# Kernel optimization log

Hardware: AMD Instinct MI355X
Metric: run time of the kernel (lower is better)

## Reference

```python
import jax, jax.numpy as jnp
import numpy as np

N_SUBJECTS, C_IN, C_OUT = 128, 273, 273
B, T = 256, 360


def setup_inputs() -> dict:
    key = jax.random.key(0)
    k1, k2, k3 = jax.random.split(key, 3)
    x = jax.random.normal(k1, (B, C_IN, T), dtype=jnp.float32)
    subjects = jax.random.randint(k2, (B,), 0, N_SUBJECTS, dtype=jnp.int64)
    weights = jax.random.normal(k3, (N_SUBJECTS, C_IN, C_OUT), dtype=jnp.float32)
    return {"x": x, "subjects": subjects, "weights": weights}


def reference(x, subjects, weights):
    # Gather per-sample weight matrix: (B, C, D)
    w = weights[subjects]
    # bct,bcd -> bdt : per-sample channel remap applied at every timestep
    return jnp.einsum('bct,bcd->bdt', x, w)
```

## Files before the change

kernel.cpp:

```cpp
#include <hip/hip_runtime.h>
#include <hip/hip_bf16.h>

#define NBATCH 256
#define NC 273
#define ND 273
#define NT 360
#define NSUB 128

#define THREADS 512
#define BM 288
#define BN 192
#define BK 32
#define LDK 40
#define KITERS 9

#define WT_LD 288
#define WT_SUBJ (288 * 288)
#define WT_BYTES ((size_t)NSUB * WT_SUBJ * 2)

typedef __bf16 bf16_t;
typedef bf16_t bf16x4 __attribute__((ext_vector_type(4)));
typedef bf16_t bf16x8 __attribute__((ext_vector_type(8)));
typedef float  f32x4  __attribute__((ext_vector_type(4)));

#define LDS_FENCE_BARRIER()                                   \
    do {                                                      \
        asm volatile("s_waitcnt lgkmcnt(0)" ::: "memory");    \
        __builtin_amdgcn_s_barrier();                         \
    } while (0)

__global__ __launch_bounds__(256) void conv_w(const float* __restrict__ w,
                                              bf16_t* __restrict__ wT) {
    const int bid  = blockIdx.x;
    const int s    = bid / 25;
    const int tile = bid % 25;
    const int c0   = (tile / 5) * 64;
    const int d0   = (tile % 5) * 64;
    const int tx   = threadIdx.x & 63;
    const int ty   = threadIdx.x >> 6;

    __shared__ float t[64][65];
    const float* __restrict__ wsrc = w + (size_t)s * NC * ND;
#pragma unroll
    for (int j = 0; j < 16; ++j) {
        const int row = ty + j * 4;
        const int c = c0 + row, d = d0 + tx;
        t[row][tx] = (c < NC && d < ND) ? wsrc[c * ND + d] : 0.f;
    }
    __syncthreads();
    bf16_t* __restrict__ wdst = wT + (size_t)s * WT_SUBJ;
#pragma unroll
    for (int j = 0; j < 16; ++j) {
        const int row = ty + j * 4;
        const int d = d0 + row, c = c0 + tx;
        if (d < ND && c < WT_LD)
            wdst[d * WT_LD + c] = (bf16_t)t[tx][row];
    }
}

template<bool BF16W>
__global__ __launch_bounds__(THREADS, 2) void subject_gemm(
    const float*  __restrict__ x,
    const int*    __restrict__ subjects,
    const float*  __restrict__ w,
    const bf16_t* __restrict__ wT,
    float*        __restrict__ out)
{
    const int raw  = blockIdx.x;
    const int xcd  = raw & 7;
    const int slot = raw >> 3;
    const int b    = xcd * 32 + (slot >> 1);
    const int tt   = slot & 1;
    const int t0   = tt * BN;
    const int bnv  = tt ? (NT - BN) : BN;
    const int s    = subjects[b];

    const float*  __restrict__ xb  = x  + (size_t)b * NC * NT;
    const float*  __restrict__ wsf = w  + (size_t)s * NC * ND;
    const bf16_t* __restrict__ wsb = wT + (size_t)s * WT_SUBJ;

    __shared__ __align__(16) bf16_t As[2][BM * LDK];
    __shared__ __align__(16) bf16_t Bs[2][BN * LDK];

    const int tid   = threadIdx.x;
    const int lane  = tid & 63;
    const int wid   = tid >> 6;
    const int wm    = wid >> 2;
    const int wn    = wid & 3;
    const int l16   = lane & 15;
    const int khalf = lane >> 4;

    int offA[5], gA[5], dA[5], cqA[5];
#pragma unroll
    for (int j = 0; j < 5; ++j) {
        const int i  = tid + THREADS * j;
        const int ii = (i < 2304) ? i : 2303;
        const int kq = ii & 7;
        const int d  = ii >> 3;
        offA[j] = d * LDK + kq * 4;
        gA[j]   = d * WT_LD + kq * 4;
        dA[j]   = d;
        cqA[j]  = kq * 4;
    }
    int offB[3], gB[3];
#pragma unroll
    for (int j = 0; j < 3; ++j) {
        const int i  = tid + THREADS * j;
        const int t  = i % BN;
        const int kq = i / BN;
        const int tc = (t < bnv) ? t : (bnv - 1);
        offB[j] = t * LDK + kq * 4;
        gB[j]   = kq * 4 * NT + t0 + tc;
    }
    const bool haveJ4 = (tid < 2304 - 4 * THREADS);

    bf16x4 aEv[5], aOd[5];
    float  bEv[3][4], bOd[3][4];

    auto loadA = [&](bf16x4 (&r)[5], int kk) {
        if constexpr (BF16W) {
#pragma unroll
            for (int j = 0; j < 4; ++j)
                r[j] = *(const bf16x4*)&wsb[gA[j] + kk];
            if (haveJ4)
                r[4] = *(const bf16x4*)&wsb[gA[4] + kk];
        } else {
#pragma unroll
            for (int j = 0; j < 5; ++j) {
                if (j == 4 && !haveJ4) break;
                bf16x4 v;
#pragma unroll
                for (int u = 0; u < 4; ++u) {
                    const int c = kk + cqA[j] + u;
                    const float f = (c < NC && dA[j] < ND) ? wsf[c * ND + dA[j]] : 0.f;
                    v[u] = (bf16_t)f;
                }
                r[j] = v;
            }
        }
    };
    auto loadB = [&](float (&r)[3][4], int kk) {
        const int base = kk * NT;
#pragma unroll
        for (int j = 0; j < 3; ++j)
#pragma unroll
            for (int u = 0; u < 4; ++u)
                r[j][u] = xb[base + gB[j] + u * NT];
    };
    auto loadB_tail = [&](float (&r)[3][4]) {
#pragma unroll
        for (int j = 0; j < 3; ++j) {
#pragma unroll
            for (int u = 0; u < 4; ++u) {
                const int c  = 256 + (gB[j] / NT)  + u;
                const int cc = (c < NC) ? c : (NC - 1);
                r[j][u] = xb[cc * NT + (gB[j] % NT)];
            }
        }
    };
    auto stage = [&](const bf16x4 (&rA)[5], const float (&rB)[3][4],
                     bf16_t* dA_, bf16_t* dB_) {
#pragma unroll
        for (int j = 0; j < 4; ++j)
            *(bf16x4*)&dA_[offA[j]] = rA[j];
        if (haveJ4)
            *(bf16x4*)&dA_[offA[4]] = rA[4];
#pragma unroll
        for (int j = 0; j < 3; ++j) {
            bf16x4 v;
#pragma unroll
            for (int u = 0; u < 4; ++u) v[u] = (bf16_t)rB[j][u];
            *(bf16x4*)&dB_[offB[j]] = v;
        }
    };

    f32x4 acc[9][3];
#pragma unroll
    for (int m = 0; m < 9; ++m)
#pragma unroll
        for (int n = 0; n < 3; ++n)
            acc[m][n] = (f32x4){0.f, 0.f, 0.f, 0.f};

    loadA(aEv, 0);       loadB(bEv, 0);
    loadA(aOd, BK);      loadB(bOd, BK);
    stage(aEv, bEv, &As[0][0], &Bs[0][0]);
    LDS_FENCE_BARRIER();

#pragma unroll
    for (int p = 0; p < 4; ++p) {
        {
            const int it0 = 2 * p;
            bf16x8 af[9], bfr[3];
#pragma unroll
            for (int n = 0; n < 3; ++n)
                bfr[n] = *(const bf16x8*)&Bs[0][(wn * 48 + n * 16 + l16) * LDK + khalf * 8];
#pragma unroll
            for (int m = 0; m < 9; ++m)
                af[m] = *(const bf16x8*)&As[0][(wm * 144 + m * 16 + l16) * LDK + khalf * 8];

            if (it0 + 2 <= KITERS - 2) {
                loadA(aEv, (it0 + 2) * BK);
                loadB(bEv, (it0 + 2) * BK);
            } else {
                loadA(aEv, 256);
                loadB_tail(bEv);
            }
            stage(aOd, bOd, &As[1][0], &Bs[1][0]);
            LDS_FENCE_BARRIER();

#pragma unroll
            for (int m = 0; m < 9; ++m)
#pragma unroll
                for (int n = 0; n < 3; ++n)
                    acc[m][n] = __builtin_amdgcn_mfma_f32_16x16x32_bf16(af[m], bfr[n], acc[m][n], 0, 0, 0);
        }
        {
            const int it1 = 2 * p + 1;
            bf16x8 af[9], bfr[3];
#pragma unroll
            for (int n = 0; n < 3; ++n)
                bfr[n] = *(const bf16x8*)&Bs[1][(wn * 48 + n * 16 + l16) * LDK + khalf * 8];
#pragma unroll
            for (int m = 0; m < 9; ++m)
                af[m] = *(const bf16x8*)&As[1][(wm * 144 + m * 16 + l16) * LDK + khalf * 8];

            if (it1 + 2 <= KITERS - 2) {
                loadA(aOd, (it1 + 2) * BK);
                loadB(bOd, (it1 + 2) * BK);
            }
            stage(aEv, bEv, &As[0][0], &Bs[0][0]);
            LDS_FENCE_BARRIER();

#pragma unroll
            for (int m = 0; m < 9; ++m)
#pragma unroll
                for (int n = 0; n < 3; ++n)
                    acc[m][n] = __builtin_amdgcn_mfma_f32_16x16x32_bf16(af[m], bfr[n], acc[m][n], 0, 0, 0);
        }
    }
    {
        bf16x8 af[9], bfr[3];
#pragma unroll
        for (int n = 0; n < 3; ++n)
            bfr[n] = *(const bf16x8*)&Bs[0][(wn * 48 + n * 16 + l16) * LDK + khalf * 8];
#pragma unroll
        for (int m = 0; m < 9; ++m)
            af[m] = *(const bf16x8*)&As[0][(wm * 144 + m * 16 + l16) * LDK + khalf * 8];
#pragma unroll
        for (int m = 0; m < 9; ++m)
#pragma unroll
            for (int n = 0; n < 3; ++n)
                acc[m][n] = __builtin_amdgcn_mfma_f32_16x16x32_bf16(af[m], bfr[n], acc[m][n], 0, 0, 0);
    }

    float* __restrict__ ob = out + (size_t)b * ND * NT;
#pragma unroll
    for (int m = 0; m < 9; ++m) {
#pragma unroll
        for (int n = 0; n < 3; ++n) {
            const int tc = wn * 48 + n * 16 + l16;
            const int gt = t0 + tc;
#pragma unroll
            for (int rg = 0; rg < 4; ++rg) {
                const int d = wm * 144 + m * 16 + khalf * 4 + rg;
                if (d < ND && tc < bnv)
                    ob[(size_t)d * NT + gt] = acc[m][n][rg];
            }
        }
    }
}

extern "C" void kernel_launch(void* const* d_in, const int* in_sizes, int n_in,
                              void* d_out, int out_size, void* d_ws, size_t ws_size,
                              hipStream_t stream) {
    const float* x        = (const float*)d_in[0];
    const int*   subjects = (const int*)d_in[1];
    const float* w        = (const float*)d_in[2];
    float*       out      = (float*)d_out;
    bf16_t*      wT       = (bf16_t*)d_ws;

    const int nblocks = NBATCH * 2;

    if (ws_size >= WT_BYTES) {
        conv_w<<<NSUB * 25, 256, 0, stream>>>(w, wT);
        subject_gemm<true><<<nblocks, THREADS, 0, stream>>>(x, subjects, w, wT, out);
    } else {
        subject_gemm<false><<<nblocks, THREADS, 0, stream>>>(x, subjects, w, wT, out);
    }
}
```

Baseline: 70.20 us.

## Shrink time tile to 64 and use six blocks per sample

Cuts the time-dimension tile from 192 to 64, splits each sample into six tiles instead of two, and raises the launch-bounds occupancy hint to 4 blocks per CU. The per-thread register footprint drops (9 accumulators instead of 27, single prefetch set), and the pipeline becomes a one-stage register prefetch with the LDS store placed after the MFMAs. This targets the low occupancy and the poor grid fill of 512 large blocks. The cost is reloading the full 288x273 weight tile three times as often per sample and a lower MFMA-to-load ratio.

```diff
diff --git a/kernel.cpp b/kernel.cpp
--- a/kernel.cpp
+++ b/kernel.cpp
@@ -9,7 +9,7 @@
 
 #define THREADS 512
 #define BM 288
-#define BN 192
+#define BN 64
 #define BK 32
 #define LDK 40
 #define KITERS 9
@@ -59,7 +59,7 @@
 }
 
 template<bool BF16W>
-__global__ __launch_bounds__(THREADS, 2) void subject_gemm(
+__global__ __launch_bounds__(THREADS, 4) void subject_gemm(
     const float*  __restrict__ x,
     const int*    __restrict__ subjects,
     const float*  __restrict__ w,
@@ -69,10 +69,10 @@
     const int raw  = blockIdx.x;
     const int xcd  = raw & 7;
     const int slot = raw >> 3;
-    const int b    = xcd * 32 + (slot >> 1);
-    const int tt   = slot & 1;
+    const int b    = xcd * 32 + slot / 6;
+    const int tt   = slot % 6;
     const int t0   = tt * BN;
-    const int bnv  = tt ? (NT - BN) : BN;
+    const int bnv  = (tt == 5) ? (NT - 5 * BN) : BN;
     const int s    = subjects[b];
 
     const float*  __restrict__ xb  = x  + (size_t)b * NC * NT;
@@ -102,28 +102,24 @@
         dA[j]   = d;
         cqA[j]  = kq * 4;
     }
-    int offB[3], gB[3];
-#pragma unroll
-    for (int j = 0; j < 3; ++j) {
-        const int i  = tid + THREADS * j;
-        const int t  = i % BN;
-        const int kq = i / BN;
-        const int tc = (t < bnv) ? t : (bnv - 1);
-        offB[j] = t * LDK + kq * 4;
-        gB[j]   = kq * 4 * NT + t0 + tc;
-    }
     const bool haveJ4 = (tid < 2304 - 4 * THREADS);
 
-    bf16x4 aEv[5], aOd[5];
-    float  bEv[3][4], bOd[3][4];
-
-    auto loadA = [&](bf16x4 (&r)[5], int kk) {
+    const int tB   = lane;
+    const int kqB  = wid;
+    const int tcB  = (tB < bnv) ? tB : (bnv - 1);
+    const int offB = tB * LDK + kqB * 4;
+    const int gBb  = kqB * 4 * NT + t0 + tcB;
+
+    bf16x4 aS[5];
+    float  bS[4];
+
+    auto loadA = [&](int kk) {
         if constexpr (BF16W) {
 #pragma unroll
             for (int j = 0; j < 4; ++j)
-                r[j] = *(const bf16x4*)&wsb[gA[j] + kk];
+                aS[j] = *(const bf16x4*)&wsb[gA[j] + kk];
             if (haveJ4)
-                r[4] = *(const bf16x4*)&wsb[gA[4] + kk];
+                aS[4] = *(const bf16x4*)&wsb[gA[4] + kk];
         } else {
 #pragma unroll
             for (int j = 0; j < 5; ++j) {
@@ -135,137 +131,88 @@
                     const float f = (c < NC && dA[j] < ND) ? wsf[c * ND + dA[j]] : 0.f;
                     v[u] = (bf16_t)f;
                 }
-                r[j] = v;
+                aS[j] = v;
             }
         }
     };
-    auto loadB = [&](float (&r)[3][4], int kk) {
+    auto loadB = [&](int kk) {
         const int base = kk * NT;
 #pragma unroll
-        for (int j = 0; j < 3; ++j)
-#pragma unroll
-            for (int u = 0; u < 4; ++u)
-                r[j][u] = xb[base + gB[j] + u * NT];
+        for (int u = 0; u < 4; ++u)
+            bS[u] = xb[base + gBb + u * NT];
     };
-    auto loadB_tail = [&](float (&r)[3][4]) {
-#pragma unroll
-        for (int j = 0; j < 3; ++j) {
-#pragma unroll
-            for (int u = 0; u < 4; ++u) {
-                const int c  = 256 + (gB[j] / NT)  + u;
-                const int cc = (c < NC) ? c : (NC - 1);
-                r[j][u] = xb[cc * NT + (gB[j] % NT)];
-            }
+    auto loadB_tail = [&]() {
+#pragma unroll
+        for (int u = 0; u < 4; ++u) {
+            const int c  = 256 + kqB * 4 + u;
+            const int cc = (c < NC) ? c : (NC - 1);
+            bS[u] = xb[cc * NT + t0 + tcB];
         }
     };
-    auto stage = [&](const bf16x4 (&rA)[5], const float (&rB)[3][4],
-                     bf16_t* dA_, bf16_t* dB_) {
-#pragma unroll
-        for (int j = 0; j < 4; ++j)
-            *(bf16x4*)&dA_[offA[j]] = rA[j];
-        if (haveJ4)
-            *(bf16x4*)&dA_[offA[4]] = rA[4];
-#pragma unroll
-        for (int j = 0; j < 3; ++j) {
-            bf16x4 v;
-#pragma unroll
-            for (int u = 0; u < 4; ++u) v[u] = (bf16_t)rB[j][u];
-            *(bf16x4*)&dB_[offB[j]] = v;
-        }
-    };
-
-    f32x4 acc[9][3];
+
+    f32x4 acc[9];
 #pragma unroll
     for (int m = 0; m < 9; ++m)
-#pragma unroll
-        for (int n = 0; n < 3; ++n)
-            acc[m][n] = (f32x4){0.f, 0.f, 0.f, 0.f};
-
-    loadA(aEv, 0);       loadB(bEv, 0);
-    loadA(aOd, BK);      loadB(bOd, BK);
-    stage(aEv, bEv, &As[0][0], &Bs[0][0]);
+        acc[m] = (f32x4){0.f, 0.f, 0.f, 0.f};
+
+    loadA(0);
+    loadB(0);
+    {
+#pragma unroll
+        for (int j = 0; j < 4; ++j) *(bf16x4*)&As[0][offA[j]] = aS[j];
+        if (haveJ4)                 *(bf16x4*)&As[0][offA[4]] = aS[4];
+        bf16x4 v;
+#pragma unroll
+        for (int u = 0; u < 4; ++u) v[u] = (bf16_t)bS[u];
+        *(bf16x4*)&Bs[0][offB] = v;
+    }
     LDS_FENCE_BARRIER();
 
-#pragma unroll
-    for (int p = 0; p < 4; ++p) {
-        {
-            const int it0 = 2 * p;
-            bf16x8 af[9], bfr[3];
-#pragma unroll
-            for (int n = 0; n < 3; ++n)
-                bfr[n] = *(const bf16x8*)&Bs[0][(wn * 48 + n * 16 + l16) * LDK + khalf * 8];
-#pragma unroll
-            for (int m = 0; m < 9; ++m)
-                af[m] = *(const bf16x8*)&As[0][(wm * 144 + m * 16 + l16) * LDK + khalf * 8];
-
-            if (it0 + 2 <= KITERS - 2) {
-                loadA(aEv, (it0 + 2) * BK);
-                loadB(bEv, (it0 + 2) * BK);
-            } else {
-                loadA(aEv, 256);
-                loadB_tail(bEv);
-            }
-            stage(aOd, bOd, &As[1][0], &Bs[1][0]);
-            LDS_FENCE_BARRIER();
-
-#pragma unroll
-            for (int m = 0; m < 9; ++m)
-#pragma unroll
-                for (int n = 0; n < 3; ++n)
-                    acc[m][n] = __builtin_amdgcn_mfma_f32_16x16x32_bf16(af[m], bfr[n], acc[m][n], 0, 0, 0);
-        }
-        {
-            const int it1 = 2 * p + 1;
-            bf16x8 af[9], bfr[3];
-#pragma unroll
-            for (int n = 0; n < 3; ++n)
-                bfr[n] = *(const bf16x8*)&Bs[1][(wn * 48 + n * 16 + l16) * LDK + khalf * 8];
-#pragma unroll
-            for (int m = 0; m < 9; ++m)
-                af[m] = *(const bf16x8*)&As[1][(wm * 144 + m * 16 + l16) * LDK + khalf * 8];
-
-            if (it1 + 2 <= KITERS - 2) {
-                loadA(aOd, (it1 + 2) * BK);
-                loadB(bOd, (it1 + 2) * BK);
-            }
-            stage(aEv, bEv, &As[0][0], &Bs[0][0]);
-            LDS_FENCE_BARRIER();
-
-#pragma unroll
-            for (int m = 0; m < 9; ++m)
-#pragma unroll
-                for (int n = 0; n < 3; ++n)
-                    acc[m][n] = __builtin_amdgcn_mfma_f32_16x16x32_bf16(af[m], bfr[n], acc[m][n], 0, 0, 0);
-        }
-    }
-    {
-        bf16x8 af[9], bfr[3];
-#pragma unroll
-        for (int n = 0; n < 3; ++n)
-            bfr[n] = *(const bf16x8*)&Bs[0][(wn * 48 + n * 16 + l16) * LDK + khalf * 8];
-#pragma unroll
-        for (int m = 0; m < 9; ++m)
-            af[m] = *(const bf16x8*)&As[0][(wm * 144 + m * 16 + l16) * LDK + khalf * 8];
-#pragma unroll
-        for (int m = 0; m < 9; ++m)
-#pragma unroll
-            for (int n = 0; n < 3; ++n)
-                acc[m][n] = __builtin_amdgcn_mfma_f32_16x16x32_bf16(af[m], bfr[n], acc[m][n], 0, 0, 0);
-    }
+#define GEMM_ITER(IT, RD, WR)                                                          \
+    {                                                                                  \
+        bf16x8 af[9];                                                                  \
+        const bf16x8 bfr = *(const bf16x8*)&Bs[RD][(wn * 16 + l16) * LDK + khalf * 8]; \
+        _Pragma("unroll")                                                              \
+        for (int m = 0; m < 9; ++m)                                                    \
+            af[m] = *(const bf16x8*)&As[RD][(wm * 144 + m * 16 + l16) * LDK + khalf * 8]; \
+        if ((IT) < KITERS - 2)      { loadA(((IT) + 1) * BK); loadB(((IT) + 1) * BK); } \
+        else if ((IT) == KITERS - 2){ loadA(256);             loadB_tail(); }          \
+        _Pragma("unroll")                                                              \
+        for (int m = 0; m < 9; ++m)                                                    \
+            acc[m] = __builtin_amdgcn_mfma_f32_16x16x32_bf16(af[m], bfr, acc[m], 0, 0, 0); \
+        if ((IT) < KITERS - 1) {                                                       \
+            _Pragma("unroll")                                                          \
+            for (int j = 0; j < 4; ++j) *(bf16x4*)&As[WR][offA[j]] = aS[j];            \
+            if (haveJ4)                 *(bf16x4*)&As[WR][offA[4]] = aS[4];             \
+            bf16x4 v;                                                                  \
+            _Pragma("unroll")                                                          \
+            for (int u = 0; u < 4; ++u) v[u] = (bf16_t)bS[u];                          \
+            *(bf16x4*)&Bs[WR][offB] = v;                                               \
+            LDS_FENCE_BARRIER();                                                       \
+        }                                                                              \
+    }
+
+    GEMM_ITER(0, 0, 1)
+    GEMM_ITER(1, 1, 0)
+    GEMM_ITER(2, 0, 1)
+    GEMM_ITER(3, 1, 0)
+    GEMM_ITER(4, 0, 1)
+    GEMM_ITER(5, 1, 0)
+    GEMM_ITER(6, 0, 1)
+    GEMM_ITER(7, 1, 0)
+    GEMM_ITER(8, 0, 1)
+#undef GEMM_ITER
 
     float* __restrict__ ob = out + (size_t)b * ND * NT;
+    const int tc = wn * 16 + l16;
+    const int gt = t0 + tc;
 #pragma unroll
     for (int m = 0; m < 9; ++m) {
 #pragma unroll
-        for (int n = 0; n < 3; ++n) {
-            const int tc = wn * 48 + n * 16 + l16;
-            const int gt = t0 + tc;
-#pragma unroll
-            for (int rg = 0; rg < 4; ++rg) {
-                const int d = wm * 144 + m * 16 + khalf * 4 + rg;
-                if (d < ND && tc < bnv)
-                    ob[(size_t)d * NT + gt] = acc[m][n][rg];
-            }
+        for (int rg = 0; rg < 4; ++rg) {
+            const int d = wm * 144 + m * 16 + khalf * 4 + rg;
+            if (d < ND && tc < bnv)
+                ob[(size_t)d * NT + gt] = acc[m][rg];
         }
     }
 }
@@ -279,7 +226,7 @@
     float*       out      = (float*)d_out;
     bf16_t*      wT       = (bf16_t*)d_ws;
 
-    const int nblocks = NBATCH * 2;
+    const int nblocks = NBATCH * 6;
 
     if (ws_size >= WT_BYTES) {
         conv_w<<<NSUB * 25, 256, 0, stream>>>(w, wT);
```

Result: slower. 78.09 us (+11.2%).
